# Optimization experiments

Measured on AMD Instinct MI355X. Metric: run time of the kernel, lower is better.

The kernel has to match this reference:

```python
import jax, jax.numpy as jnp
import numpy as np

B, C, L, D, H = 8, 64, 128, 768, 768  # batch, candidates, tokens, hidden, mlp hidden


def setup_inputs() -> dict:
    key = jax.random.key(0)
    k0, k1, k2 = jax.random.split(key, 3)
    inp = jax.random.normal(k0, (B, C, 2, L, D), dtype=jnp.float32)
    # MlpModule params (input_size = 768*2): Linear(2D->H) -> ReLU -> Linear(H->1)
    W1 = jax.random.normal(k1, (2 * D, H), dtype=jnp.float32) * 0.02
    b1 = jnp.zeros((H,), dtype=jnp.float32)
    W2 = jax.random.normal(k2, (H, 1), dtype=jnp.float32) * 0.02
    b2 = jnp.zeros((1,), dtype=jnp.float32)
    return {"input": inp, "W1": W1, "b1": b1, "W2": W2, "b2": b2}


def reference(input, W1, b1, W2, b2):
    b, c, _, l, d = input.shape
    context = input[:, :, 0].reshape(b * c, l, d)  # [BC, L, D]
    entity = input[:, :, 1].reshape(b * c, l, d)   # [BC, L, D]
    mask = (context[:, :, 0] != 0).astype(context.dtype)  # [BC, L]

    # bmm similarity: [BC, L, L]
    sim = jnp.einsum('bld,bmd->blm', context, entity)
    dot_scores = jnp.max(sim, axis=-1)          # [BC, L]
    argmax_values = jnp.argmax(sim, axis=-1)    # [BC, L]

    # gather best-matching entity token per context token: [BC, L, D]
    gathered = jnp.take_along_axis(entity, argmax_values[..., None], axis=1)

    # MLP over stacked (context, entity) pair -> flatten to 2D features
    mlp_in = jnp.concatenate([context, gathered], axis=-1)  # [BC, L, 2D]
    h = jax.nn.relu(mlp_in @ W1 + b1)
    scores = (h @ W2 + b2)[..., 0]              # [BC, L]

    scores = jnp.sum(scores * mask, axis=-1)              # [BC]
    dot_scores = jnp.sum(dot_scores * mask, axis=-1).reshape(b, c)  # [B, C]
    return scores, dot_scores
```

## Files before the change

### kernel.cpp

```cpp
#include <hip/hip_runtime.h>
#include <hip/hip_bf16.h>
#include <stdint.h>

#define NPAIR 512
#define LTOK  128
#define DDIM  768
#define HDIM  768
#define K2    1536
#define MARGIN 0.4f

typedef float f32x4 __attribute__((ext_vector_type(4)));
typedef short bf16x8 __attribute__((ext_vector_type(8)));

static __device__ __forceinline__ int fsw(int row) {
    return (row ^ (row >> 2)) & 3;
}

static __device__ __forceinline__ unsigned short f2bf(float f) {
    union { float f; uint32_t u; } v; v.f = f;
    uint32_t u = v.u;
    u += 0x7FFF + ((u >> 16) & 1);
    return (unsigned short)(u >> 16);
}

static __device__ __forceinline__ uint2 pack4(f32x4 v) {
    __hip_bfloat162 lo = __float22bfloat162_rn(float2{v[0], v[1]});
    __hip_bfloat162 hi = __float22bfloat162_rn(float2{v[2], v[3]});
    uint2 r;
    r.x = *reinterpret_cast<unsigned*>(&lo);
    r.y = *reinterpret_cast<unsigned*>(&hi);
    return r;
}

static __device__ __forceinline__ uint4 pack8(f32x4 a, f32x4 b) {
    uint2 lo = pack4(a), hi = pack4(b);
    uint4 r; r.x = lo.x; r.y = lo.y; r.z = hi.x; r.w = hi.y;
    return r;
}

typedef const __attribute__((address_space(1))) void* gas_t;
typedef __attribute__((address_space(3))) void* las_t;
static __device__ __forceinline__ void gld16(const void* g, void* l) {
    __builtin_amdgcn_global_load_lds((gas_t)g, (las_t)l, 16, 0, 0);
}

static __device__ __forceinline__ float wave_dot(const float* __restrict__ a,
                                                 const float* __restrict__ b,
                                                 int lane) {
    f32x4 s4 = {0.f, 0.f, 0.f, 0.f};
#pragma unroll
    for (int it = 0; it < 3; ++it) {
        int k = it * 256 + lane * 4;
        f32x4 av = *(const f32x4*)(a + k);
        f32x4 bv = *(const f32x4*)(b + k);
#pragma unroll
        for (int q = 0; q < 4; ++q) s4[q] = fmaf(av[q], bv[q], s4[q]);
    }
    float v = (s4[0] + s4[1]) + (s4[2] + s4[3]);
#pragma unroll
    for (int m = 1; m < 64; m <<= 1) v += __shfl_xor(v, m);
    return v;
}

__global__ __launch_bounds__(512, 4) void fused_kernel(
        const float* __restrict__ inp,
        const unsigned short* __restrict__ W1T,
        const float* __restrict__ b1,
        const float* __restrict__ W2,
        const float* __restrict__ b2,
        unsigned short* __restrict__ Cbf, unsigned short* __restrict__ Ebf,
        float* __restrict__ out)
{
    const int p    = blockIdx.x;
    const int t    = threadIdx.x;
    const int wv   = t >> 6;
    const int lane = t & 63;
    const int s    = lane & 15, g = lane >> 4;

    const float* Cbase = inp + (size_t)(2 * p) * LTOK * DDIM;
    const float* Ebase = Cbase + (size_t)LTOK * DDIM;

    __shared__ char  pool[49152];
    __shared__ int   am[128];
    __shared__ float dm[128];
    __shared__ float tok[128];

    unsigned short (*Cl)[128][32] = (unsigned short (*)[128][32])pool;
    unsigned short (*El)[128][32] = (unsigned short (*)[128][32])(pool + 16384);
    unsigned short (*cand)[16]    = (unsigned short (*)[16])(pool + 32768);
    int*   ccnt = (int*)(pool + 36864);
    float* rm1  = (float*)(pool + 37376);
    int*   ri1  = (int*)(pool + 37888);

    if (t < 128) { ccnt[t] = 0; tok[t] = 0.f; }

    f32x4 acc1[8];
#pragma unroll
    for (int j = 0; j < 8; j++) acc1[j] = (f32x4){0.f, 0.f, 0.f, 0.f};

    const int srow0 = t >> 3;
    const int srow1 = 64 + srow0;
    const int so8   = t & 7;
    const int sh    = so8 >> 2;
    const int sq    = so8 & 3;
    const int qs0   = (sq ^ fsw(srow0)) * 8;
    const int qs1   = (sq ^ fsw(srow1)) * 8;

    f32x4 cbuf[4], ebuf[4];

    auto ISSUE = [&](int kc) {
        const int k0 = kc * 64;
        const float* c0a = Cbase + (size_t)srow0 * DDIM + k0 + so8 * 8;
        const float* c1a = Cbase + (size_t)srow1 * DDIM + k0 + so8 * 8;
        const float* e0a = Ebase + (size_t)srow0 * DDIM + k0 + so8 * 8;
        const float* e1a = Ebase + (size_t)srow1 * DDIM + k0 + so8 * 8;
        cbuf[0] = *(const f32x4*)c0a;  cbuf[1] = *(const f32x4*)(c0a + 4);
        cbuf[2] = *(const f32x4*)c1a;  cbuf[3] = *(const f32x4*)(c1a + 4);
        ebuf[0] = *(const f32x4*)e0a;  ebuf[1] = *(const f32x4*)(e0a + 4);
        ebuf[2] = *(const f32x4*)e1a;  ebuf[3] = *(const f32x4*)(e1a + 4);
    };

    ISSUE(0);
    for (int kc = 0; kc < 12; ++kc) {
        const int k0 = kc * 64;
        uint4 cw0 = pack8(cbuf[0], cbuf[1]);
        uint4 cw1 = pack8(cbuf[2], cbuf[3]);
        uint4 ew0 = pack8(ebuf[0], ebuf[1]);
        uint4 ew1 = pack8(ebuf[2], ebuf[3]);
        *(uint4*)&Cl[sh][srow0][qs0] = cw0;
        *(uint4*)&Cl[sh][srow1][qs1] = cw1;
        *(uint4*)&El[sh][srow0][qs0] = ew0;
        *(uint4*)&El[sh][srow1][qs1] = ew1;
        __syncthreads();

        if (kc < 11) ISSUE(kc + 1);
        {
            size_t o0 = ((size_t)p * LTOK + srow0) * DDIM + k0 + so8 * 8;
            size_t o1 = ((size_t)p * LTOK + srow1) * DDIM + k0 + so8 * 8;
            *(uint4*)(Cbf + o0) = cw0;
            *(uint4*)(Cbf + o1) = cw1;
            *(uint4*)(Ebf + o0) = ew0;
            *(uint4*)(Ebf + o1) = ew1;
        }

#pragma unroll
        for (int h = 0; h < 2; ++h) {
            const int arow = wv * 16 + s;
            bf16x8 af = *(const bf16x8*)&Cl[h][arow][(g ^ fsw(arow)) * 8];
            bf16x8 bfr[8];
#pragma unroll
            for (int j = 0; j < 8; ++j) {
                const int row = j * 16 + s;
                bfr[j] = *(const bf16x8*)&El[h][row][(g ^ fsw(row)) * 8];
            }
#pragma unroll
            for (int j = 0; j < 8; ++j)
                acc1[j] = __builtin_amdgcn_mfma_f32_16x16x32_bf16(af, bfr[j], acc1[j], 0, 0, 0);
        }
        __syncthreads();
    }

#pragma unroll
    for (int r = 0; r < 4; ++r) {
        float m1 = acc1[0][r]; int i1 = s; float m2 = -1e30f;
#pragma unroll
        for (int j = 1; j < 8; ++j) {
            float v = acc1[j][r]; int c = j * 16 + s;
            if (v > m1 || (v == m1 && c < i1)) { m2 = m1; m1 = v; i1 = c; }
            else if (v > m2) m2 = v;
        }
#pragma unroll
        for (int msk = 1; msk < 16; msk <<= 1) {
            float o1 = __shfl_xor(m1, msk);
            int   oi = __shfl_xor(i1, msk);
            float o2 = __shfl_xor(m2, msk);
            bool take = (o1 > m1) || (o1 == m1 && oi < i1);
            float nm2 = take ? fmaxf(m1, o2) : fmaxf(m2, o1);
            if (take) { m1 = o1; i1 = oi; }
            m2 = nm2;
        }
        int row = wv * 16 + g * 4 + r;
        if (s == 0) { rm1[row] = m1; ri1[row] = i1; }
        float thr = m1 - MARGIN;
#pragma unroll
        for (int j = 0; j < 8; ++j) {
            float v = acc1[j][r]; int c = j * 16 + s;
            if (v >= thr && c != i1) {
                int idx = atomicAdd(&ccnt[row], 1);
                if (idx < 16) cand[row][idx] = (unsigned short)c;
            }
        }
    }
    __syncthreads();

    for (int rr = 0; rr < 16; ++rr) {
        int row = wv + rr * 8;
        int cnt = ccnt[row];
        float m1 = rm1[row]; int i1 = ri1[row];
        if (cnt == 0) {
            if (lane == 0) { dm[row] = m1; am[row] = i1; }
            continue;
        }
        const float* cr = Cbase + (size_t)row * DDIM;
        float bv; int bc;
        if (cnt <= 16) {
            bv = wave_dot(cr, Ebase + (size_t)i1 * DDIM, lane); bc = i1;
            for (int q = 0; q < cnt; ++q) {
                int c = cand[row][q];
                float v = wave_dot(cr, Ebase + (size_t)c * DDIM, lane);
                if (v > bv || (v == bv && c < bc)) { bv = v; bc = c; }
            }
        } else {
            bv = -1e30f; bc = 0;
            for (int c = 0; c < 128; ++c) {
                float v = wave_dot(cr, Ebase + (size_t)c * DDIM, lane);
                if (v > bv || (v == bv && c < bc)) { bv = v; bc = c; }
            }
        }
        if (lane == 0) { dm[row] = bv; am[row] = bc; }
    }
    __syncthreads();

    unsigned short (*Ald)[128][32] = (unsigned short (*)[128][32])pool;
    unsigned short (*Bld)[256][32] = (unsigned short (*)[256][32])(pool + 16384);

    const int wr  = wv >> 2, wcg = wv & 3;
    const int rsub = lane >> 2;
    const int chk  = lane & 3;

    for (int cb = 0; cb < 3; ++cb) {
        f32x4 acc[4][4];
#pragma unroll
        for (int i = 0; i < 4; i++)
#pragma unroll
            for (int j = 0; j < 4; j++) acc[i][j] = (f32x4){0.f, 0.f, 0.f, 0.f};

        auto STAGE = [&](int buf, int kt) {
            const int k0   = kt * 32;
            const bool ctx = (kt < 24);
            const int kloc = ctx ? k0 : (k0 - DDIM);
#pragma unroll
            for (int n = 0; n < 2; ++n) {
                int r0  = (wv * 2 + n) * 16;
                int col = r0 + rsub;
                int ck  = chk ^ fsw(col);
                gld16(W1T + (size_t)(cb * 256 + col) * K2 + k0 + ck * 8,
                      &Bld[buf][r0][0]);
            }
            {
                int r0 = wv * 16;
                int r  = r0 + rsub;
                int ck = chk ^ fsw(r);
                const unsigned short* base = ctx
                    ? (Cbf + ((size_t)p * LTOK + r) * DDIM)
                    : (Ebf + ((size_t)p * LTOK + am[r]) * DDIM);
                gld16(base + kloc + ck * 8, &Ald[buf][r0][0]);
            }
        };

        STAGE(0, 0);
        __syncthreads();
        int cur = 0;
        for (int kt = 0; kt < 48; ++kt) {
            if (kt < 47) STAGE(cur ^ 1, kt + 1);
            bf16x8 af[4], bfr[4];
#pragma unroll
            for (int i = 0; i < 4; ++i) {
                const int row = wr * 64 + i * 16 + s;
                af[i] = *(const bf16x8*)&Ald[cur][row][(g ^ fsw(row)) * 8];
            }
#pragma unroll
            for (int j = 0; j < 4; ++j) {
                const int brow = wcg * 64 + j * 16 + s;
                bfr[j] = *(const bf16x8*)&Bld[cur][brow][(g ^ fsw(brow)) * 8];
            }
#pragma unroll
            for (int i = 0; i < 4; ++i)
#pragma unroll
                for (int j = 0; j < 4; ++j)
                    acc[i][j] = __builtin_amdgcn_mfma_f32_16x16x32_bf16(af[i], bfr[j], acc[i][j], 0, 0, 0);
            __syncthreads();
            cur ^= 1;
        }

        float w2v[4], b1v[4];
#pragma unroll
        for (int j = 0; j < 4; j++) {
            int col = cb * 256 + wcg * 64 + j * 16 + s;
            w2v[j] = W2[col];
            b1v[j] = b1[col];
        }
        float ss[4][4];
#pragma unroll
        for (int i = 0; i < 4; i++)
#pragma unroll
            for (int r = 0; r < 4; r++) ss[i][r] = 0.f;
#pragma unroll
        for (int i = 0; i < 4; i++)
#pragma unroll
            for (int j = 0; j < 4; j++)
#pragma unroll
                for (int r = 0; r < 4; r++) {
                    float h = acc[i][j][r] + b1v[j];
                    h = h > 0.f ? h : 0.f;
                    ss[i][r] = fmaf(h, w2v[j], ss[i][r]);
                }
#pragma unroll
        for (int sft = 1; sft < 16; sft <<= 1)
#pragma unroll
            for (int i = 0; i < 4; i++)
#pragma unroll
                for (int r = 0; r < 4; r++) ss[i][r] += __shfl_xor(ss[i][r], sft);
        if (s == 0) {
#pragma unroll
            for (int i = 0; i < 4; i++)
#pragma unroll
                for (int r = 0; r < 4; r++)
                    atomicAdd(&tok[wr * 64 + i * 16 + g * 4 + r], ss[i][r]);
        }
    }
    __syncthreads();

    if (wv == 0) {
        float b2v = b2[0];
        float sc = 0.f, dd = 0.f;
#pragma unroll
        for (int rr = 0; rr < 2; ++rr) {
            int row = lane + rr * 64;
            float c0 = Cbase[(size_t)row * DDIM];
            float mk = (c0 != 0.f) ? 1.f : 0.f;
            sc += mk * (tok[row] + b2v);
            dd += mk * dm[row];
        }
#pragma unroll
        for (int m = 1; m < 64; m <<= 1) {
            sc += __shfl_xor(sc, m);
            dd += __shfl_xor(dd, m);
        }
        if (lane == 0) { out[p] = sc; out[NPAIR + p] = dd; }
    }
}

__global__ __launch_bounds__(256) void w1t_kernel(
        const float* __restrict__ W1, unsigned short* __restrict__ W1T)
{
    int idx = blockIdx.x * 256 + threadIdx.x;
    if (idx >= HDIM * K2 / 8) return;
    int c  = idx / (K2 / 8);
    int k0 = (idx % (K2 / 8)) * 8;
    unsigned short v[8];
#pragma unroll
    for (int q = 0; q < 8; q++) v[q] = f2bf(W1[(size_t)(k0 + q) * HDIM + c]);
    *(uint4*)(W1T + (size_t)c * K2 + k0) = *(const uint4*)v;
}

__global__ __launch_bounds__(256) void sim_fp32_kernel(
        const float* __restrict__ inp,
        float* __restrict__ dotmax, int* __restrict__ argmax)
{
    const int p  = blockIdx.x;
    const int t  = threadIdx.x;
    const int tx = t & 15, ty = t >> 4;
    const float* Cbase = inp + (size_t)(2 * p) * LTOK * DDIM;
    const float* Ebase = Cbase + (size_t)LTOK * DDIM;

    __shared__ float Ct[128][36];
    __shared__ float Et[128][36];

    float acc[8][8];
#pragma unroll
    for (int i = 0; i < 8; i++)
#pragma unroll
        for (int j = 0; j < 8; j++) acc[i][j] = 0.f;

    for (int kc = 0; kc < 24; ++kc) {
        const int k0 = kc * 32;
#pragma unroll
        for (int q = 0; q < 4; ++q) {
            int f = q * 256 + t;
            int row = f >> 3, c4 = f & 7;
            *(f32x4*)&Ct[row][c4 * 4] = *(const f32x4*)(Cbase + (size_t)row * DDIM + k0 + c4 * 4);
            *(f32x4*)&Et[row][c4 * 4] = *(const f32x4*)(Ebase + (size_t)row * DDIM + k0 + c4 * 4);
        }
        __syncthreads();
#pragma unroll
        for (int kk4 = 0; kk4 < 8; ++kk4) {
            f32x4 cr[8], er[8];
#pragma unroll
            for (int i = 0; i < 8; i++) cr[i] = *(const f32x4*)&Ct[ty + 16 * i][kk4 * 4];
#pragma unroll
            for (int j = 0; j < 8; j++) er[j] = *(const f32x4*)&Et[tx + 16 * j][kk4 * 4];
#pragma unroll
            for (int kk = 0; kk < 4; kk++)
#pragma unroll
                for (int i = 0; i < 8; i++)
#pragma unroll
                    for (int j = 0; j < 8; j++)
                        acc[i][j] = fmaf(cr[i][kk], er[j][kk], acc[i][j]);
        }
        __syncthreads();
    }
#pragma unroll
    for (int i = 0; i < 8; i++) {
        float m = acc[i][0]; int mi = tx;
#pragma unroll
        for (int j = 1; j < 8; j++) {
            int c = tx + 16 * j;
            float v = acc[i][j];
            if (v > m || (v == m && c < mi)) { m = v; mi = c; }
        }
#pragma unroll
        for (int sft = 1; sft < 16; sft <<= 1) {
            float vo = __shfl_xor(m, sft);
            int   io = __shfl_xor(mi, sft);
            if (vo > m || (vo == m && io < mi)) { m = vo; mi = io; }
        }
        if (tx == 0) {
            int r = ty + 16 * i;
            dotmax[(size_t)p * LTOK + r] = m;
            argmax[(size_t)p * LTOK + r] = mi;
        }
    }
}

__global__ __launch_bounds__(256, 2) void mlp_kernel(
        const float* __restrict__ inp,
        const unsigned short* __restrict__ W1T,
        const float* __restrict__ b1,
        const float* __restrict__ W2,
        const int* __restrict__ argmax,
        float* __restrict__ tokscore)
{
    const int tile = blockIdx.x;
    const int cb   = blockIdx.y;
    const int t    = threadIdx.x;
    const int wv   = t >> 6;
    const int lane = t & 63;
    const int s    = lane & 15, g = lane >> 4;

    __shared__ unsigned short At[64][32];
    __shared__ unsigned short Bt[384][32];
    __shared__ int am[64];

    if (t < 64) am[t] = argmax[tile * 64 + t];
    __syncthreads();

    f32x4 acc[4][6];
#pragma unroll
    for (int i = 0; i < 4; i++)
#pragma unroll
        for (int j = 0; j < 6; j++) acc[i][j] = (f32x4){0.f, 0.f, 0.f, 0.f};

    for (int kc = 0; kc < 48; ++kc) {
        const int k0  = kc * 32;
        const int sel = (kc >= 24) ? 1 : 0;
        const int kloc = k0 - sel * DDIM;
#pragma unroll
        for (int q = 0; q < 2; ++q) {
            int f = q * 256 + t;
            int row = f >> 3, c4 = f & 7;
            int token = tile * 64 + row;
            int pp = token >> 7;
            int lsel = sel ? am[row] : (token & 127);
            const float* src = inp + ((size_t)(2 * pp + sel) * LTOK + lsel) * DDIM + kloc + c4 * 4;
            f32x4 v = *(const f32x4*)src;
            uint2 pk = pack4(v);
            *(uint2*)&At[row][c4 * 4] = pk;
        }
#pragma unroll
        for (int q = 0; q < 6; ++q) {
            int f = q * 256 + t;
            int colr = f >> 2, q8 = f & 3;
            const unsigned short* src = W1T + (size_t)(cb * 384 + colr) * K2 + k0 + q8 * 8;
            *(uint4*)&Bt[colr][q8 * 8] = *(const uint4*)src;
        }
        __syncthreads();

        bf16x8 af[4], bfr[6];
#pragma unroll
        for (int i = 0; i < 4; i++) af[i]  = *(const bf16x8*)&At[i * 16 + s][g * 8];
#pragma unroll
        for (int j = 0; j < 6; j++) bfr[j] = *(const bf16x8*)&Bt[wv * 96 + j * 16 + s][g * 8];
#pragma unroll
        for (int i = 0; i < 4; i++)
#pragma unroll
            for (int j = 0; j < 6; j++)
                acc[i][j] = __builtin_amdgcn_mfma_f32_16x16x32_bf16(af[i], bfr[j], acc[i][j], 0, 0, 0);
        __syncthreads();
    }

    float w2v[6], b1v[6];
#pragma unroll
    for (int j = 0; j < 6; j++) {
        int col = cb * 384 + wv * 96 + j * 16 + s;
        w2v[j] = W2[col];
        b1v[j] = b1[col];
    }
    float ssum[4][4];
#pragma unroll
    for (int i = 0; i < 4; i++)
#pragma unroll
        for (int r = 0; r < 4; r++) ssum[i][r] = 0.f;
#pragma unroll
    for (int i = 0; i < 4; i++)
#pragma unroll
        for (int j = 0; j < 6; j++)
#pragma unroll
            for (int r = 0; r < 4; r++) {
                float h = acc[i][j][r] + b1v[j];
                h = h > 0.f ? h : 0.f;
                ssum[i][r] = fmaf(h, w2v[j], ssum[i][r]);
            }
#pragma unroll
    for (int sft = 1; sft < 16; sft <<= 1)
#pragma unroll
        for (int i = 0; i < 4; i++)
#pragma unroll
            for (int r = 0; r < 4; r++) ssum[i][r] += __shfl_xor(ssum[i][r], sft);
    if (s == 0) {
#pragma unroll
        for (int i = 0; i < 4; i++)
#pragma unroll
            for (int r = 0; r < 4; r++)
                atomicAdd(&tokscore[tile * 64 + i * 16 + g * 4 + r], ssum[i][r]);
    }
}

__global__ __launch_bounds__(128) void reduce_kernel(
        const float* __restrict__ inp,
        const float* __restrict__ tokscore,
        const float* __restrict__ dotmax,
        const float* __restrict__ b2,
        float* __restrict__ out)
{
    int p = blockIdx.x;
    int l = threadIdx.x;
    float c0  = inp[((size_t)(2 * p) * LTOK + l) * DDIM];
    float msk = (c0 != 0.0f) ? 1.f : 0.f;
    float sc  = (tokscore[p * LTOK + l] + b2[0]) * msk;
    float dm  = dotmax[p * LTOK + l] * msk;
#pragma unroll
    for (int sh = 1; sh < 64; sh <<= 1) {
        sc += __shfl_xor(sc, sh);
        dm += __shfl_xor(dm, sh);
    }
    __shared__ float tmp[4];
    if ((l & 63) == 0) { tmp[(l >> 6) * 2] = sc; tmp[(l >> 6) * 2 + 1] = dm; }
    __syncthreads();
    if (l == 0) {
        out[p]          = tmp[0] + tmp[2];
        out[NPAIR + p]  = tmp[1] + tmp[3];
    }
}

extern "C" void kernel_launch(void* const* d_in, const int* in_sizes, int n_in,
                              void* d_out, int out_size, void* d_ws, size_t ws_size,
                              hipStream_t stream)
{
    const float* inp = (const float*)d_in[0];
    const float* W1  = (const float*)d_in[1];
    const float* b1  = (const float*)d_in[2];
    const float* W2  = (const float*)d_in[3];
    const float* b2  = (const float*)d_in[4];
    float* out = (float*)d_out;

    char* ws = (char*)d_ws;
    unsigned short* W1T   = (unsigned short*)ws;
    float*          dotmx = (float*)(ws + 2359296);
    int*            amax  = (int*)(ws + 2359296 + 262144);
    float*          toksc = (float*)(ws + 2359296 + 2*262144);
    unsigned short* Cbf   = (unsigned short*)(ws + 2359296 + 3*262144);
    unsigned short* Ebf   = Cbf + (size_t)NPAIR * LTOK * DDIM;
    const size_t NEED = 2359296ull + 3ull*262144ull + 2ull*100663296ull;

    const bool big = ws_size >= NEED;

    w1t_kernel<<<(HDIM * K2 / 8 + 255) / 256, 256, 0, stream>>>(W1, W1T);
    if (big) {
        fused_kernel<<<NPAIR, 512, 0, stream>>>(inp, W1T, b1, W2, b2, Cbf, Ebf, out);
    } else {
        hipMemsetAsync(toksc, 0, 65536 * sizeof(float), stream);
        sim_fp32_kernel<<<NPAIR, 256, 0, stream>>>(inp, dotmx, amax);
        mlp_kernel<<<dim3(1024, 2), 256, 0, stream>>>(inp, W1T, b1, W2, amax, toksc);
        reduce_kernel<<<NPAIR, 128, 0, stream>>>(inp, toksc, dotmx, b2, out);
    }
}
```

Before: 303.8 us.

## Split fused kernel across two context-row halves per pair with finalize pass

The fused kernel now launches two blocks per pair, each handling 64 of the 128 context tokens against all entity tokens. Similarity, argmax refinement and the MLP all run on half-height tiles, and a small finalize kernel sums the two partial results. The aim is more blocks and better occupancy and load balance across CUs. The cost is that each block reloads and re-converts the full entity matrix (redundant reads and Ebf writes) and pays for an extra launch. The MLP staging also leaves half the waves idle while A is loaded.

```diff
diff --git a/kernel.cpp b/kernel.cpp
--- a/kernel.cpp
+++ b/kernel.cpp
@@ -62,16 +62,17 @@
     return v;
 }
 
-__global__ __launch_bounds__(512, 4) void fused_kernel(
+__global__ __launch_bounds__(512, 4) void fused2_kernel(
         const float* __restrict__ inp,
         const unsigned short* __restrict__ W1T,
         const float* __restrict__ b1,
         const float* __restrict__ W2,
         const float* __restrict__ b2,
         unsigned short* __restrict__ Cbf, unsigned short* __restrict__ Ebf,
-        float* __restrict__ out)
+        float* __restrict__ pp)
 {
-    const int p    = blockIdx.x;
+    const int h    = blockIdx.x;
+    const int p    = blockIdx.y;
     const int t    = threadIdx.x;
     const int wv   = t >> 6;
     const int lane = t & 63;
@@ -80,81 +81,78 @@
     const float* Cbase = inp + (size_t)(2 * p) * LTOK * DDIM;
     const float* Ebase = Cbase + (size_t)LTOK * DDIM;
 
-    __shared__ char  pool[49152];
-    __shared__ int   am[128];
-    __shared__ float dm[128];
-    __shared__ float tok[128];
-
-    unsigned short (*Cl)[128][32] = (unsigned short (*)[128][32])pool;
-    unsigned short (*El)[128][32] = (unsigned short (*)[128][32])(pool + 16384);
-    unsigned short (*cand)[16]    = (unsigned short (*)[16])(pool + 32768);
-    int*   ccnt = (int*)(pool + 36864);
-    float* rm1  = (float*)(pool + 37376);
-    int*   ri1  = (int*)(pool + 37888);
-
-    if (t < 128) { ccnt[t] = 0; tok[t] = 0.f; }
-
-    f32x4 acc1[8];
-#pragma unroll
-    for (int j = 0; j < 8; j++) acc1[j] = (f32x4){0.f, 0.f, 0.f, 0.f};
-
-    const int srow0 = t >> 3;
-    const int srow1 = 64 + srow0;
+    __shared__ char  pool[40960];
+    __shared__ int   am[64];
+    __shared__ float dm[64];
+    __shared__ float tok[64];
+    __shared__ float rm1[64];
+    __shared__ int   ri1[64];
+
+    unsigned short (*Cl)[64][32]  = (unsigned short (*)[64][32])pool;
+    unsigned short (*El)[128][32] = (unsigned short (*)[128][32])(pool + 8192);
+    unsigned short (*cand)[16]    = (unsigned short (*)[16])(pool + 24576);
+    int*   ccnt = (int*)(pool + 26624);
+    float* hm1  = (float*)(pool + 26880);
+    int*   hi1  = (int*)(pool + 27392);
+
+    f32x4 acc1[4];
+#pragma unroll
+    for (int j = 0; j < 4; j++) acc1[j] = (f32x4){0.f, 0.f, 0.f, 0.f};
+
+    const int crow  = t >> 3;
+    const int erow0 = t >> 3;
+    const int erow1 = 64 + erow0;
     const int so8   = t & 7;
-    const int sh    = so8 >> 2;
+    const int shh   = so8 >> 2;
     const int sq    = so8 & 3;
-    const int qs0   = (sq ^ fsw(srow0)) * 8;
-    const int qs1   = (sq ^ fsw(srow1)) * 8;
-
-    f32x4 cbuf[4], ebuf[4];
+    const int qc    = (sq ^ fsw(crow))  * 8;
+    const int qe0   = (sq ^ fsw(erow0)) * 8;
+    const int qe1   = (sq ^ fsw(erow1)) * 8;
+
+    f32x4 cb2[2], eb[4];
 
     auto ISSUE = [&](int kc) {
         const int k0 = kc * 64;
-        const float* c0a = Cbase + (size_t)srow0 * DDIM + k0 + so8 * 8;
-        const float* c1a = Cbase + (size_t)srow1 * DDIM + k0 + so8 * 8;
-        const float* e0a = Ebase + (size_t)srow0 * DDIM + k0 + so8 * 8;
-        const float* e1a = Ebase + (size_t)srow1 * DDIM + k0 + so8 * 8;
-        cbuf[0] = *(const f32x4*)c0a;  cbuf[1] = *(const f32x4*)(c0a + 4);
-        cbuf[2] = *(const f32x4*)c1a;  cbuf[3] = *(const f32x4*)(c1a + 4);
-        ebuf[0] = *(const f32x4*)e0a;  ebuf[1] = *(const f32x4*)(e0a + 4);
-        ebuf[2] = *(const f32x4*)e1a;  ebuf[3] = *(const f32x4*)(e1a + 4);
+        const float* ca  = Cbase + (size_t)(h * 64 + crow) * DDIM + k0 + so8 * 8;
+        const float* e0a = Ebase + (size_t)erow0 * DDIM + k0 + so8 * 8;
+        const float* e1a = Ebase + (size_t)erow1 * DDIM + k0 + so8 * 8;
+        cb2[0] = *(const f32x4*)ca;   cb2[1] = *(const f32x4*)(ca + 4);
+        eb[0]  = *(const f32x4*)e0a;  eb[1]  = *(const f32x4*)(e0a + 4);
+        eb[2]  = *(const f32x4*)e1a;  eb[3]  = *(const f32x4*)(e1a + 4);
     };
+
+    const int rt = wv >> 1, ch = wv & 1;
 
     ISSUE(0);
     for (int kc = 0; kc < 12; ++kc) {
         const int k0 = kc * 64;
-        uint4 cw0 = pack8(cbuf[0], cbuf[1]);
-        uint4 cw1 = pack8(cbuf[2], cbuf[3]);
-        uint4 ew0 = pack8(ebuf[0], ebuf[1]);
-        uint4 ew1 = pack8(ebuf[2], ebuf[3]);
-        *(uint4*)&Cl[sh][srow0][qs0] = cw0;
-        *(uint4*)&Cl[sh][srow1][qs1] = cw1;
-        *(uint4*)&El[sh][srow0][qs0] = ew0;
-        *(uint4*)&El[sh][srow1][qs1] = ew1;
+        uint4 cw  = pack8(cb2[0], cb2[1]);
+        uint4 ew0 = pack8(eb[0], eb[1]);
+        uint4 ew1 = pack8(eb[2], eb[3]);
+        *(uint4*)&Cl[shh][crow][qc]   = cw;
+        *(uint4*)&El[shh][erow0][qe0] = ew0;
+        *(uint4*)&El[shh][erow1][qe1] = ew1;
         __syncthreads();
 
         if (kc < 11) ISSUE(kc + 1);
         {
-            size_t o0 = ((size_t)p * LTOK + srow0) * DDIM + k0 + so8 * 8;
-            size_t o1 = ((size_t)p * LTOK + srow1) * DDIM + k0 + so8 * 8;
-            *(uint4*)(Cbf + o0) = cw0;
-            *(uint4*)(Cbf + o1) = cw1;
-            *(uint4*)(Ebf + o0) = ew0;
-            *(uint4*)(Ebf + o1) = ew1;
-        }
-
-#pragma unroll
-        for (int h = 0; h < 2; ++h) {
-            const int arow = wv * 16 + s;
-            bf16x8 af = *(const bf16x8*)&Cl[h][arow][(g ^ fsw(arow)) * 8];
-            bf16x8 bfr[8];
-#pragma unroll
-            for (int j = 0; j < 8; ++j) {
-                const int row = j * 16 + s;
-                bfr[j] = *(const bf16x8*)&El[h][row][(g ^ fsw(row)) * 8];
-            }
-#pragma unroll
-            for (int j = 0; j < 8; ++j)
+            *(uint4*)(Cbf + ((size_t)p * LTOK + h * 64 + crow) * DDIM + k0 + so8 * 8) = cw;
+            *(uint4*)(Ebf + ((size_t)p * LTOK + erow0) * DDIM + k0 + so8 * 8) = ew0;
+            *(uint4*)(Ebf + ((size_t)p * LTOK + erow1) * DDIM + k0 + so8 * 8) = ew1;
+        }
+
+#pragma unroll
+        for (int hh = 0; hh < 2; ++hh) {
+            const int arow = rt * 16 + s;
+            bf16x8 af = *(const bf16x8*)&Cl[hh][arow][(g ^ fsw(arow)) * 8];
+            bf16x8 bfr[4];
+#pragma unroll
+            for (int j = 0; j < 4; ++j) {
+                const int brow = ch * 64 + j * 16 + s;
+                bfr[j] = *(const bf16x8*)&El[hh][brow][(g ^ fsw(brow)) * 8];
+            }
+#pragma unroll
+            for (int j = 0; j < 4; ++j)
                 acc1[j] = __builtin_amdgcn_mfma_f32_16x16x32_bf16(af, bfr[j], acc1[j], 0, 0, 0);
         }
         __syncthreads();
@@ -162,38 +160,50 @@
 
 #pragma unroll
     for (int r = 0; r < 4; ++r) {
-        float m1 = acc1[0][r]; int i1 = s; float m2 = -1e30f;
-#pragma unroll
-        for (int j = 1; j < 8; ++j) {
-            float v = acc1[j][r]; int c = j * 16 + s;
-            if (v > m1 || (v == m1 && c < i1)) { m2 = m1; m1 = v; i1 = c; }
-            else if (v > m2) m2 = v;
+        float m1 = acc1[0][r]; int i1 = ch * 64 + s;
+#pragma unroll
+        for (int j = 1; j < 4; ++j) {
+            float v = acc1[j][r]; int c = ch * 64 + j * 16 + s;
+            if (v > m1 || (v == m1 && c < i1)) { m1 = v; i1 = c; }
         }
 #pragma unroll
         for (int msk = 1; msk < 16; msk <<= 1) {
             float o1 = __shfl_xor(m1, msk);
             int   oi = __shfl_xor(i1, msk);
-            float o2 = __shfl_xor(m2, msk);
-            bool take = (o1 > m1) || (o1 == m1 && oi < i1);
-            float nm2 = take ? fmaxf(m1, o2) : fmaxf(m2, o1);
-            if (take) { m1 = o1; i1 = oi; }
-            m2 = nm2;
-        }
-        int row = wv * 16 + g * 4 + r;
-        if (s == 0) { rm1[row] = m1; ri1[row] = i1; }
-        float thr = m1 - MARGIN;
-#pragma unroll
-        for (int j = 0; j < 8; ++j) {
-            float v = acc1[j][r]; int c = j * 16 + s;
-            if (v >= thr && c != i1) {
-                int idx = atomicAdd(&ccnt[row], 1);
-                if (idx < 16) cand[row][idx] = (unsigned short)c;
-            }
-        }
+            if (o1 > m1 || (o1 == m1 && oi < i1)) { m1 = o1; i1 = oi; }
+        }
+        int rowl = rt * 16 + g * 4 + r;
+        if (s == 0) { hm1[ch * 64 + rowl] = m1; hi1[ch * 64 + rowl] = i1; }
     }
     __syncthreads();
 
-    for (int rr = 0; rr < 16; ++rr) {
+    if (t < 64) {
+        float a = hm1[t]; int ia = hi1[t];
+        float b = hm1[64 + t]; int ib = hi1[64 + t];
+        bool bw = (b > a);
+        rm1[t] = bw ? b : a;
+        ri1[t] = bw ? ib : ia;
+        ccnt[t] = 0; tok[t] = 0.f;
+    }
+    __syncthreads();
+
+#pragma unroll
+    for (int r = 0; r < 4; ++r) {
+        int rowl = rt * 16 + g * 4 + r;
+        float thr = rm1[rowl] - MARGIN;
+        int i1g = ri1[rowl];
+#pragma unroll
+        for (int j = 0; j < 4; ++j) {
+            float v = acc1[j][r]; int c = ch * 64 + j * 16 + s;
+            if (v >= thr && c != i1g) {
+                int idx = atomicAdd(&ccnt[rowl], 1);
+                if (idx < 16) cand[rowl][idx] = (unsigned short)c;
+            }
+        }
+    }
+    __syncthreads();
+
+    for (int rr = 0; rr < 8; ++rr) {
         int row = wv + rr * 8;
         int cnt = ccnt[row];
         float m1 = rm1[row]; int i1 = ri1[row];
@@ -201,7 +211,7 @@
             if (lane == 0) { dm[row] = m1; am[row] = i1; }
             continue;
         }
-        const float* cr = Cbase + (size_t)row * DDIM;
+        const float* cr = Cbase + (size_t)(h * 64 + row) * DDIM;
         float bv; int bc;
         if (cnt <= 16) {
             bv = wave_dot(cr, Ebase + (size_t)i1 * DDIM, lane); bc = i1;
@@ -221,17 +231,17 @@
     }
     __syncthreads();
 
-    unsigned short (*Ald)[128][32] = (unsigned short (*)[128][32])pool;
-    unsigned short (*Bld)[256][32] = (unsigned short (*)[256][32])(pool + 16384);
-
-    const int wr  = wv >> 2, wcg = wv & 3;
+    unsigned short (*Ald)[64][32]  = (unsigned short (*)[64][32])pool;
+    unsigned short (*Bld)[256][32] = (unsigned short (*)[256][32])(pool + 8192);
+
+    const int rt2 = wv >> 2, cq = wv & 3;
     const int rsub = lane >> 2;
     const int chk  = lane & 3;
 
     for (int cb = 0; cb < 3; ++cb) {
-        f32x4 acc[4][4];
-#pragma unroll
-        for (int i = 0; i < 4; i++)
+        f32x4 acc[2][4];
+#pragma unroll
+        for (int i = 0; i < 2; i++)
 #pragma unroll
             for (int j = 0; j < 4; j++) acc[i][j] = (f32x4){0.f, 0.f, 0.f, 0.f};
 
@@ -247,12 +257,12 @@
                 gld16(W1T + (size_t)(cb * 256 + col) * K2 + k0 + ck * 8,
                       &Bld[buf][r0][0]);
             }
-            {
+            if (wv < 4) {
                 int r0 = wv * 16;
                 int r  = r0 + rsub;
                 int ck = chk ^ fsw(r);
                 const unsigned short* base = ctx
-                    ? (Cbf + ((size_t)p * LTOK + r) * DDIM)
+                    ? (Cbf + ((size_t)p * LTOK + h * 64 + r) * DDIM)
                     : (Ebf + ((size_t)p * LTOK + am[r]) * DDIM);
                 gld16(base + kloc + ck * 8, &Ald[buf][r0][0]);
             }
@@ -263,19 +273,19 @@
         int cur = 0;
         for (int kt = 0; kt < 48; ++kt) {
             if (kt < 47) STAGE(cur ^ 1, kt + 1);
-            bf16x8 af[4], bfr[4];
-#pragma unroll
-            for (int i = 0; i < 4; ++i) {
-                const int row = wr * 64 + i * 16 + s;
+            bf16x8 af[2], bfr[4];
+#pragma unroll
+            for (int i = 0; i < 2; ++i) {
+                const int row = rt2 * 32 + i * 16 + s;
                 af[i] = *(const bf16x8*)&Ald[cur][row][(g ^ fsw(row)) * 8];
             }
 #pragma unroll
             for (int j = 0; j < 4; ++j) {
-                const int brow = wcg * 64 + j * 16 + s;
+                const int brow = cq * 64 + j * 16 + s;
                 bfr[j] = *(const bf16x8*)&Bld[cur][brow][(g ^ fsw(brow)) * 8];
             }
 #pragma unroll
-            for (int i = 0; i < 4; ++i)
+            for (int i = 0; i < 2; ++i)
 #pragma unroll
                 for (int j = 0; j < 4; ++j)
                     acc[i][j] = __builtin_amdgcn_mfma_f32_16x16x32_bf16(af[i], bfr[j], acc[i][j], 0, 0, 0);
@@ -286,59 +296,65 @@
         float w2v[4], b1v[4];
 #pragma unroll
         for (int j = 0; j < 4; j++) {
-            int col = cb * 256 + wcg * 64 + j * 16 + s;
+            int col = cb * 256 + cq * 64 + j * 16 + s;
             w2v[j] = W2[col];
             b1v[j] = b1[col];
         }
-        float ss[4][4];
-#pragma unroll
-        for (int i = 0; i < 4; i++)
+        float ss[2][4];
+#pragma unroll
+        for (int i = 0; i < 2; i++)
 #pragma unroll
             for (int r = 0; r < 4; r++) ss[i][r] = 0.f;
 #pragma unroll
-        for (int i = 0; i < 4; i++)
+        for (int i = 0; i < 2; i++)
 #pragma unroll
             for (int j = 0; j < 4; j++)
 #pragma unroll
                 for (int r = 0; r < 4; r++) {
-                    float h = acc[i][j][r] + b1v[j];
-                    h = h > 0.f ? h : 0.f;
-                    ss[i][r] = fmaf(h, w2v[j], ss[i][r]);
+                    float hh = acc[i][j][r] + b1v[j];
+                    hh = hh > 0.f ? hh : 0.f;
+                    ss[i][r] = fmaf(hh, w2v[j], ss[i][r]);
                 }
 #pragma unroll
         for (int sft = 1; sft < 16; sft <<= 1)
 #pragma unroll
-            for (int i = 0; i < 4; i++)
+            for (int i = 0; i < 2; i++)
 #pragma unroll
                 for (int r = 0; r < 4; r++) ss[i][r] += __shfl_xor(ss[i][r], sft);
         if (s == 0) {
 #pragma unroll
-            for (int i = 0; i < 4; i++)
+            for (int i = 0; i < 2; i++)
 #pragma unroll
                 for (int r = 0; r < 4; r++)
-                    atomicAdd(&tok[wr * 64 + i * 16 + g * 4 + r], ss[i][r]);
+                    atomicAdd(&tok[rt2 * 32 + i * 16 + g * 4 + r], ss[i][r]);
         }
     }
     __syncthreads();
 
     if (wv == 0) {
         float b2v = b2[0];
-        float sc = 0.f, dd = 0.f;
-#pragma unroll
-        for (int rr = 0; rr < 2; ++rr) {
-            int row = lane + rr * 64;
-            float c0 = Cbase[(size_t)row * DDIM];
-            float mk = (c0 != 0.f) ? 1.f : 0.f;
-            sc += mk * (tok[row] + b2v);
-            dd += mk * dm[row];
-        }
+        float c0 = Cbase[(size_t)(h * 64 + lane) * DDIM];
+        float mk = (c0 != 0.f) ? 1.f : 0.f;
+        float sc = mk * (tok[lane] + b2v);
+        float dd = mk * dm[lane];
 #pragma unroll
         for (int m = 1; m < 64; m <<= 1) {
             sc += __shfl_xor(sc, m);
             dd += __shfl_xor(dd, m);
         }
-        if (lane == 0) { out[p] = sc; out[NPAIR + p] = dd; }
-    }
+        if (lane == 0) {
+            pp[h * NPAIR + p]        = sc;
+            pp[1024 + h * NPAIR + p] = dd;
+        }
+    }
+}
+
+__global__ __launch_bounds__(512) void finalize_kernel(
+        const float* __restrict__ pp, float* __restrict__ out)
+{
+    int t = threadIdx.x;
+    out[t]         = pp[t] + pp[NPAIR + t];
+    out[NPAIR + t] = pp[1024 + t] + pp[1024 + NPAIR + t];
 }
 
 __global__ __launch_bounds__(256) void w1t_kernel(
@@ -460,9 +476,9 @@
             int f = q * 256 + t;
             int row = f >> 3, c4 = f & 7;
             int token = tile * 64 + row;
-            int pp = token >> 7;
+            int pp2 = token >> 7;
             int lsel = sel ? am[row] : (token & 127);
-            const float* src = inp + ((size_t)(2 * pp + sel) * LTOK + lsel) * DDIM + kloc + c4 * 4;
+            const float* src = inp + ((size_t)(2 * pp2 + sel) * LTOK + lsel) * DDIM + kloc + c4 * 4;
             f32x4 v = *(const f32x4*)src;
             uint2 pk = pack4(v);
             *(uint2*)&At[row][c4 * 4] = pk;
@@ -507,9 +523,9 @@
         for (int j = 0; j < 6; j++)
 #pragma unroll
             for (int r = 0; r < 4; r++) {
-                float h = acc[i][j][r] + b1v[j];
-                h = h > 0.f ? h : 0.f;
-                ssum[i][r] = fmaf(h, w2v[j], ssum[i][r]);
+                float hh = acc[i][j][r] + b1v[j];
+                hh = hh > 0.f ? hh : 0.f;
+                ssum[i][r] = fmaf(hh, w2v[j], ssum[i][r]);
             }
 #pragma unroll
     for (int sft = 1; sft < 16; sft <<= 1)
@@ -538,14 +554,14 @@
     float c0  = inp[((size_t)(2 * p) * LTOK + l) * DDIM];
     float msk = (c0 != 0.0f) ? 1.f : 0.f;
     float sc  = (tokscore[p * LTOK + l] + b2[0]) * msk;
-    float dm  = dotmax[p * LTOK + l] * msk;
+    float dmv = dotmax[p * LTOK + l] * msk;
 #pragma unroll
     for (int sh = 1; sh < 64; sh <<= 1) {
-        sc += __shfl_xor(sc, sh);
-        dm += __shfl_xor(dm, sh);
+        sc  += __shfl_xor(sc, sh);
+        dmv += __shfl_xor(dmv, sh);
     }
     __shared__ float tmp[4];
-    if ((l & 63) == 0) { tmp[(l >> 6) * 2] = sc; tmp[(l >> 6) * 2 + 1] = dm; }
+    if ((l & 63) == 0) { tmp[(l >> 6) * 2] = sc; tmp[(l >> 6) * 2 + 1] = dmv; }
     __syncthreads();
     if (l == 0) {
         out[p]          = tmp[0] + tmp[2];
@@ -566,6 +582,7 @@
 
     char* ws = (char*)d_ws;
     unsigned short* W1T   = (unsigned short*)ws;
+    float*          pp    = (float*)(ws + 2359296);
     float*          dotmx = (float*)(ws + 2359296);
     int*            amax  = (int*)(ws + 2359296 + 262144);
     float*          toksc = (float*)(ws + 2359296 + 2*262144);
@@ -577,7 +594,8 @@
 
     w1t_kernel<<<(HDIM * K2 / 8 + 255) / 256, 256, 0, stream>>>(W1, W1T);
     if (big) {
-        fused_kernel<<<NPAIR, 512, 0, stream>>>(inp, W1T, b1, W2, b2, Cbf, Ebf, out);
+        fused2_kernel<<<dim3(2, NPAIR), 512, 0, stream>>>(inp, W1T, b1, W2, b2, Cbf, Ebf, pp);
+        finalize_kernel<<<1, 512, 0, stream>>>(pp, out);
     } else {
         hipMemsetAsync(toksc, 0, 65536 * sizeof(float), stream);
         sim_fp32_kernel<<<NPAIR, 256, 0, stream>>>(inp, dotmx, amax);
```

After: 406.2 us. 33.7% more time.
